# Kernel optimization log

Hardware: AMD Instinct MI355X
Metric: run time of the kernel (lower is better)

The kernel has to match this reference:

```python
import jax, jax.numpy as jnp
import numpy as np

NUM, K = 5, 3  # grid intervals and spline order, as in KANLayer(num=5, k=3)

def _grid(num=NUM, k=K, lo=-1.0, hi=1.0):
    # base grid: num+1 points on [lo,hi], extended by k knots on each side (pykan extend_grid)
    h = (hi - lo) / num
    return jnp.linspace(lo - k * h, hi + k * h, num + 1 + 2 * k, dtype=jnp.float32)

def b_spline_basis(x, grid, k=K):
    # Cox-de Boor recursion, identical to pykan B_batch. x: (B, In) -> (B, In, num+k)
    xe = x[..., None]
    b = ((xe >= grid[:-1]) & (xe < grid[1:])).astype(x.dtype)  # order-0 indicators
    for d in range(1, k + 1):
        left = (xe - grid[:-(d + 1)]) / (grid[d:-1] - grid[:-(d + 1)])
        right = (grid[d + 1:] - xe) / (grid[d + 1:] - grid[1:-d])
        b = left * b[..., :-1] + right * b[..., 1:]
    return b

def kan_layer(x, coef, sb, ssp, grid):
    # x: (B, In); coef: (Out, In, nb); sb/ssp: (Out, In). mask == 1.
    basis = b_spline_basis(x, grid)                       # (B, In, nb)
    spline = jnp.einsum('big,oig->boi', basis, coef)      # per-edge spline value
    y = sb[None] * jax.nn.silu(x)[:, None, :] + ssp[None] * spline  # (B, Out, In)
    return y.sum(axis=2)                                  # (B, Out)

def setup_inputs() -> dict:
    key = jax.random.key(0)
    ks = jax.random.split(key, 3)
    B, IN, H, OUT, NB = 128, 3072, 256, 10, NUM + K
    return {
        "x": jax.random.normal(ks[0], (B, IN), jnp.float32),
        "coef1": 0.1 * jax.random.normal(ks[1], (H, IN, NB), jnp.float32),
        "scale_base1": jnp.ones((H, IN), jnp.float32),
        "scale_sp1": jnp.ones((H, IN), jnp.float32),
        "coef2": 0.1 * jax.random.normal(ks[2], (OUT, H, NB), jnp.float32),
        "scale_base2": jnp.ones((OUT, H), jnp.float32),
        "scale_sp2": jnp.ones((OUT, H), jnp.float32),
    }

def reference(x, coef1, scale_base1, scale_sp1, coef2, scale_base2, scale_sp2):
    g = _grid()
    h = kan_layer(x, coef1, scale_base1, scale_sp1, g)
    h = jax.nn.selu(h)
    return kan_layer(h, coef2, scale_base2, scale_sp2, g)
```

## Files before the change

### kernel.cpp

```cpp
#include <hip/hip_runtime.h>
#include <hip/hip_bf16.h>
#include <math.h>


#define B_DIM   128
#define IN1     3072
#define OUT1    256
#define NB      8
#define OUT2    10

#define CI      16
#define NCH     (IN1 / CI)
#define KS      6
#define LDP     200
#define BN      32

typedef short  bf16x8 __attribute__((ext_vector_type(8)));
typedef float  f32x4  __attribute__((ext_vector_type(4)));
typedef unsigned short ushort_t;

__device__ __forceinline__ ushort_t f2bf(float f) {
    union { __hip_bfloat16 h; ushort_t u; } v;
    v.h = __float2bfloat16(f);
    return v.u;
}
__device__ __forceinline__ float bf2f(ushort_t h) {
    union { float f; unsigned int u; } v; v.u = ((unsigned int)h) << 16;
    return v.f;
}

__device__ __forceinline__ void basis_silu(float x, float w[8], float& sil) {
    sil = x / (1.0f + __expf(-x));
    float u  = (x + 2.2f) * 2.5f;
    float uf = floorf(u);
    int   j  = (int)uf;
    float t  = u - uf;
    float omt = 1.0f - t;
    float t2 = t * t, t3 = t2 * t;
    float w0 = omt * omt * omt * (1.0f / 6.0f);
    float w1 = (3.0f * t3 - 6.0f * t2 + 4.0f) * (1.0f / 6.0f);
    float w2 = (-3.0f * t3 + 3.0f * t2 + 3.0f * t + 1.0f) * (1.0f / 6.0f);
    float w3 = t3 * (1.0f / 6.0f);
    bool valid = (u >= 0.0f) && (u < 11.0f);
#pragma unroll
    for (int g = 0; g < 8; ++g) {
        int m = g - j + 3;
        float v = (m == 0) ? w0 : (m == 1) ? w1 : (m == 2) ? w2 : (m == 3) ? w3 : 0.0f;
        w[g] = valid ? v : 0.0f;
    }
}

__device__ __forceinline__ float selu_f(float x) {
    const float scale = 1.0507009873554805f;
    const float alpha = 1.6732632423543772f;
    return (x > 0.0f) ? scale * x : scale * alpha * (__expf(x) - 1.0f);
}

__global__ __launch_bounds__(512) void kan_gemm(const float* __restrict__ x,
                                                const float* __restrict__ coef1,
                                                const float* __restrict__ sb1,
                                                const float* __restrict__ ssp1,
                                                ushort_t* __restrict__ partial) {
    __shared__ ushort_t Al[B_DIM][LDP];
    __shared__ ushort_t Bl[BN][LDP];
    const int tid   = threadIdx.x;
    const int o0    = blockIdx.x * BN;
    const int chunk = blockIdx.y;
    const int i0    = chunk * CI;

    {
        const int ol = tid >> 4;
        const int ii = tid & 15;
        const size_t e = (size_t)(o0 + ol) * IN1 + (i0 + ii);
        const float4 c0 = *reinterpret_cast<const float4*>(coef1 + e * NB);
        const float4 c1 = *reinterpret_cast<const float4*>(coef1 + e * NB + 4);
        const float sspv = ssp1[e];
        const float sbv  = sb1[e];
        ushort4 pa, pb, pc;
        pa.x = f2bf(c0.x * sspv); pa.y = f2bf(c0.y * sspv);
        pa.z = f2bf(c0.z * sspv); pa.w = f2bf(c0.w * sspv);
        pb.x = f2bf(c1.x * sspv); pb.y = f2bf(c1.y * sspv);
        pb.z = f2bf(c1.z * sspv); pb.w = f2bf(c1.w * sspv);
        pc.x = f2bf(sbv); pc.y = 0; pc.z = 0; pc.w = 0;
        *reinterpret_cast<ushort4*>(&Bl[ol][ii * 12 + 0]) = pa;
        *reinterpret_cast<ushort4*>(&Bl[ol][ii * 12 + 4]) = pb;
        *reinterpret_cast<ushort4*>(&Bl[ol][ii * 12 + 8]) = pc;
    }
    {
        const int b = tid >> 2;
        const int q = tid & 3;
        float4 xv = *reinterpret_cast<const float4*>(x + (size_t)b * IN1 + i0 + q * 4);
        float xa[4] = {xv.x, xv.y, xv.z, xv.w};
#pragma unroll
        for (int p = 0; p < 4; ++p) {
            const int ii = q * 4 + p;
            float bs[8], sil;
            basis_silu(xa[p], bs, sil);
            ushort4 pa, pb, pc;
            pa.x = f2bf(bs[0]); pa.y = f2bf(bs[1]); pa.z = f2bf(bs[2]); pa.w = f2bf(bs[3]);
            pb.x = f2bf(bs[4]); pb.y = f2bf(bs[5]); pb.z = f2bf(bs[6]); pb.w = f2bf(bs[7]);
            pc.x = f2bf(sil);   pc.y = 0;           pc.z = 0;           pc.w = 0;
            *reinterpret_cast<ushort4*>(&Al[b][ii * 12 + 0]) = pa;
            *reinterpret_cast<ushort4*>(&Al[b][ii * 12 + 4]) = pb;
            *reinterpret_cast<ushort4*>(&Al[b][ii * 12 + 8]) = pc;
        }
    }
    __syncthreads();

    const int w = tid >> 6, l = tid & 63;
    const int nt = w & 1, mg = w >> 1;
    const int row16 = l & 15, kg = (l >> 4) * 8;
    f32x4 acc0 = {0.f, 0.f, 0.f, 0.f};
    f32x4 acc1 = {0.f, 0.f, 0.f, 0.f};
#pragma unroll
    for (int ks = 0; ks < KS; ++ks) {
        bf16x8 bfrag = *reinterpret_cast<const bf16x8*>(&Bl[nt * 16 + row16][ks * 32 + kg]);
        bf16x8 a0 = *reinterpret_cast<const bf16x8*>(&Al[(mg * 2 + 0) * 16 + row16][ks * 32 + kg]);
        bf16x8 a1 = *reinterpret_cast<const bf16x8*>(&Al[(mg * 2 + 1) * 16 + row16][ks * 32 + kg]);
        acc0 = __builtin_amdgcn_mfma_f32_16x16x32_bf16(a0, bfrag, acc0, 0, 0, 0);
        acc1 = __builtin_amdgcn_mfma_f32_16x16x32_bf16(a1, bfrag, acc1, 0, 0, 0);
    }

    const size_t base = (size_t)chunk * (B_DIM * OUT1);
    const int col = o0 + nt * 16 + row16;
    const int rb  = (l >> 4) * 4;
#pragma unroll
    for (int r = 0; r < 4; ++r) {
        partial[base + (size_t)((mg * 2 + 0) * 16 + rb + r) * OUT1 + col] = f2bf(acc0[r]);
        partial[base + (size_t)((mg * 2 + 1) * 16 + rb + r) * OUT1 + col] = f2bf(acc1[r]);
    }
}

#define CPG (NCH / 4)

__global__ __launch_bounds__(1024) void kan_reduce_l2(const ushort_t* __restrict__ partial,
                                                      const float* __restrict__ coef2,
                                                      const float* __restrict__ sb2,
                                                      const float* __restrict__ ssp2,
                                                      float* __restrict__ out) {
    const int b = blockIdx.x;
    const int t = threadIdx.x;
    const int o = t & 255;
    const int g = t >> 8;
    const ushort_t* pp = partial + (size_t)g * CPG * (B_DIM * OUT1)
                                 + (size_t)b * OUT1 + o;
    float sum = 0.0f;
#pragma unroll 8
    for (int c = 0; c < CPG; ++c)
        sum += bf2f(pp[(size_t)c * (B_DIM * OUT1)]);

    __shared__ float hred[4][OUT1];
    hred[g][o] = sum;
    __syncthreads();
    const float hv = hred[0][o] + hred[1][o] + hred[2][o] + hred[3][o];

    const float sh = selu_f(hv);
    float w8[8], sil;
    basis_silu(sh, w8, sil);

    float accs[OUT2];
#pragma unroll
    for (int oo = 0; oo < OUT2; ++oo) {
        const float* cp = coef2 + ((size_t)oo * OUT1 + o) * NB;
        float4 c0 = *reinterpret_cast<const float4*>(cp);
        float4 c1 = *reinterpret_cast<const float4*>(cp + 4);
        float dot = w8[0] * c0.x + w8[1] * c0.y + w8[2] * c0.z + w8[3] * c0.w +
                    w8[4] * c1.x + w8[5] * c1.y + w8[6] * c1.z + w8[7] * c1.w;
        accs[oo] = sb2[oo * OUT1 + o] * sil + ssp2[oo * OUT1 + o] * dot;
    }

    __shared__ float red[16][OUT2];
    const int lane = t & 63, wv = t >> 6;
#pragma unroll
    for (int oo = 0; oo < OUT2; ++oo) {
        float v = accs[oo];
#pragma unroll
        for (int off = 32; off >= 1; off >>= 1) v += __shfl_xor(v, off, 64);
        if (lane == 0) red[wv][oo] = v;
    }
    __syncthreads();
    if (t < OUT2)
        out[b * OUT2 + t] = red[0][t] + red[1][t] + red[2][t] + red[3][t];
}

extern "C" void kernel_launch(void* const* d_in, const int* in_sizes, int n_in,
                              void* d_out, int out_size, void* d_ws, size_t ws_size,
                              hipStream_t stream) {
    const float* x     = (const float*)d_in[0];
    const float* coef1 = (const float*)d_in[1];
    const float* sb1   = (const float*)d_in[2];
    const float* ssp1  = (const float*)d_in[3];
    const float* coef2 = (const float*)d_in[4];
    const float* sb2   = (const float*)d_in[5];
    const float* ssp2  = (const float*)d_in[6];
    float* out = (float*)d_out;

    ushort_t* partial = (ushort_t*)d_ws;

    kan_gemm<<<dim3(OUT1 / BN, NCH), 512, 0, stream>>>(x, coef1, sb1, ssp1, partial);
    kan_reduce_l2<<<B_DIM, 1024, 0, stream>>>(partial, coef2, sb2, ssp2, out);
}
```

Measured before the change: 44.34 us.

## Widen K-chunks with double-buffered swizzled LDS pipeline and transposed x input

Each GEMM block now covers 48 input features in six stages of eight, with register prefetch two stages ahead and double-buffered XOR-swizzled LDS tiles. A separate transpose kernel makes x loads coalesced along the batch dimension. The chunk count drops from 192 to 64, which shrinks the partial buffer and the reduce loop, and partials are now stored in fp32 instead of bf16. The cost is an extra kernel launch, fewer GEMM blocks (512 vs 1536), and more syncs per block.

```diff
diff --git a/kernel.cpp b/kernel.cpp
--- a/kernel.cpp
+++ b/kernel.cpp
@@ -9,11 +9,13 @@
 #define NB      8
 #define OUT2    10
 
-#define CI      16
+#define CI      48
 #define NCH     (IN1 / CI)
-#define KS      6
-#define LDP     200
+#define NS      6
+#define SI      8
 #define BN      32
+#define ASTR_B  256
+#define BSTR_B  192
 
 typedef short  bf16x8 __attribute__((ext_vector_type(8)));
 typedef float  f32x4  __attribute__((ext_vector_type(4)));
@@ -23,10 +25,6 @@
     union { __hip_bfloat16 h; ushort_t u; } v;
     v.h = __float2bfloat16(f);
     return v.u;
-}
-__device__ __forceinline__ float bf2f(ushort_t h) {
-    union { float f; unsigned int u; } v; v.u = ((unsigned int)h) << 16;
-    return v.f;
 }
 
 __device__ __forceinline__ void basis_silu(float x, float w[8], float& sil) {
@@ -56,84 +54,145 @@
     return (x > 0.0f) ? scale * x : scale * alpha * (__expf(x) - 1.0f);
 }
 
-__global__ __launch_bounds__(512) void kan_gemm(const float* __restrict__ x,
+__global__ __launch_bounds__(256) void ktranspose(const float* __restrict__ x,
+                                                  float* __restrict__ xT) {
+    __shared__ float t[32][33];
+    int bx = blockIdx.x, by = blockIdx.y;
+    int tx = threadIdx.x, ty = threadIdx.y;
+#pragma unroll
+    for (int k = 0; k < 4; ++k)
+        t[ty + k * 8][tx] = x[(by * 32 + ty + k * 8) * IN1 + bx * 32 + tx];
+    __syncthreads();
+#pragma unroll
+    for (int k = 0; k < 4; ++k)
+        xT[(bx * 32 + ty + k * 8) * B_DIM + by * 32 + tx] = t[tx][ty + k * 8];
+}
+
+__global__ __launch_bounds__(512) void kan_gemm(const float* __restrict__ xT,
                                                 const float* __restrict__ coef1,
                                                 const float* __restrict__ sb1,
                                                 const float* __restrict__ ssp1,
-                                                ushort_t* __restrict__ partial) {
-    __shared__ ushort_t Al[B_DIM][LDP];
-    __shared__ ushort_t Bl[BN][LDP];
+                                                float* __restrict__ partial) {
+    __shared__ ushort_t Asm[2][B_DIM * (ASTR_B / 2)];
+    __shared__ ushort_t Bsm[2][BN * (BSTR_B / 2)];
+
     const int tid   = threadIdx.x;
     const int o0    = blockIdx.x * BN;
     const int chunk = blockIdx.y;
-    const int i0    = chunk * CI;
-
-    {
-        const int ol = tid >> 4;
-        const int ii = tid & 15;
-        const size_t e = (size_t)(o0 + ol) * IN1 + (i0 + ii);
-        const float4 c0 = *reinterpret_cast<const float4*>(coef1 + e * NB);
-        const float4 c1 = *reinterpret_cast<const float4*>(coef1 + e * NB + 4);
-        const float sspv = ssp1[e];
-        const float sbv  = sb1[e];
-        ushort4 pa, pb, pc;
-        pa.x = f2bf(c0.x * sspv); pa.y = f2bf(c0.y * sspv);
-        pa.z = f2bf(c0.z * sspv); pa.w = f2bf(c0.w * sspv);
-        pb.x = f2bf(c1.x * sspv); pb.y = f2bf(c1.y * sspv);
-        pb.z = f2bf(c1.z * sspv); pb.w = f2bf(c1.w * sspv);
-        pc.x = f2bf(sbv); pc.y = 0; pc.z = 0; pc.w = 0;
-        *reinterpret_cast<ushort4*>(&Bl[ol][ii * 12 + 0]) = pa;
-        *reinterpret_cast<ushort4*>(&Bl[ol][ii * 12 + 4]) = pb;
-        *reinterpret_cast<ushort4*>(&Bl[ol][ii * 12 + 8]) = pc;
-    }
-    {
-        const int b = tid >> 2;
-        const int q = tid & 3;
-        float4 xv = *reinterpret_cast<const float4*>(x + (size_t)b * IN1 + i0 + q * 4);
-        float xa[4] = {xv.x, xv.y, xv.z, xv.w};
-#pragma unroll
-        for (int p = 0; p < 4; ++p) {
-            const int ii = q * 4 + p;
-            float bs[8], sil;
-            basis_silu(xa[p], bs, sil);
-            ushort4 pa, pb, pc;
-            pa.x = f2bf(bs[0]); pa.y = f2bf(bs[1]); pa.z = f2bf(bs[2]); pa.w = f2bf(bs[3]);
-            pb.x = f2bf(bs[4]); pb.y = f2bf(bs[5]); pb.z = f2bf(bs[6]); pb.w = f2bf(bs[7]);
-            pc.x = f2bf(sil);   pc.y = 0;           pc.z = 0;           pc.w = 0;
-            *reinterpret_cast<ushort4*>(&Al[b][ii * 12 + 0]) = pa;
-            *reinterpret_cast<ushort4*>(&Al[b][ii * 12 + 4]) = pb;
-            *reinterpret_cast<ushort4*>(&Al[b][ii * 12 + 8]) = pc;
-        }
-    }
-    __syncthreads();
+    const int i_base = chunk * CI;
+
+    const int bq  = tid >> 3;
+    const int iiA = tid & 7;
+    const int ol  = (tid & 255) >> 3;
+    const int iiW = tid & 7;
+    const bool doW = (tid < 256);
 
     const int w = tid >> 6, l = tid & 63;
     const int nt = w & 1, mg = w >> 1;
-    const int row16 = l & 15, kg = (l >> 4) * 8;
+    const int row16 = l & 15, k16 = l >> 4;
+
+    float  xv0[2], xv1[2];
+    float4 c0r[2], c1r[2];
+    float  sspr[2], sbr[2];
+
+#define LOADS(set, ss)                                                          \
+    {                                                                           \
+        const int ib = i_base + (ss) * SI;                                      \
+        xv0[set] = xT[(size_t)(ib + iiA) * B_DIM + bq];                         \
+        xv1[set] = xT[(size_t)(ib + iiA) * B_DIM + bq + 64];                    \
+        if (doW) {                                                              \
+            const size_t e = (size_t)(o0 + ol) * IN1 + (ib + iiW);              \
+            c0r[set] = *reinterpret_cast<const float4*>(coef1 + e * NB);        \
+            c1r[set] = *reinterpret_cast<const float4*>(coef1 + e * NB + 4);    \
+            sspr[set] = ssp1[e];                                                \
+            sbr[set]  = sb1[e];                                                 \
+        }                                                                       \
+    }
+
     f32x4 acc0 = {0.f, 0.f, 0.f, 0.f};
     f32x4 acc1 = {0.f, 0.f, 0.f, 0.f};
-#pragma unroll
-    for (int ks = 0; ks < KS; ++ks) {
-        bf16x8 bfrag = *reinterpret_cast<const bf16x8*>(&Bl[nt * 16 + row16][ks * 32 + kg]);
-        bf16x8 a0 = *reinterpret_cast<const bf16x8*>(&Al[(mg * 2 + 0) * 16 + row16][ks * 32 + kg]);
-        bf16x8 a1 = *reinterpret_cast<const bf16x8*>(&Al[(mg * 2 + 1) * 16 + row16][ks * 32 + kg]);
-        acc0 = __builtin_amdgcn_mfma_f32_16x16x32_bf16(a0, bfrag, acc0, 0, 0, 0);
-        acc1 = __builtin_amdgcn_mfma_f32_16x16x32_bf16(a1, bfrag, acc1, 0, 0, 0);
-    }
-
-    const size_t base = (size_t)chunk * (B_DIM * OUT1);
+
+    LOADS(0, 0)
+    LOADS(1, 1)
+
+#pragma unroll
+    for (int s = 0; s < NS; ++s) {
+        const int set = s & 1;
+        char* Aw = (char*)&Asm[set][0];
+        char* Bw = (char*)&Bsm[set][0];
+
+        {
+            float xa[2] = {xv0[set], xv1[set]};
+#pragma unroll
+            for (int p = 0; p < 2; ++p) {
+                const int b = bq + p * 64;
+                float bs[8], sil;
+                basis_silu(xa[p], bs, sil);
+                ushort4 pa, pb, pc;
+                pa.x = f2bf(bs[0]); pa.y = f2bf(bs[1]); pa.z = f2bf(bs[2]); pa.w = f2bf(bs[3]);
+                pb.x = f2bf(bs[4]); pb.y = f2bf(bs[5]); pb.z = f2bf(bs[6]); pb.w = f2bf(bs[7]);
+                pc.x = f2bf(sil);   pc.y = 0;           pc.z = 0;           pc.w = 0;
+                char* rowp = Aw + b * ASTR_B;
+                const int sw = (b & 7) << 4;
+                *reinterpret_cast<ushort4*>(rowp + ((iiA * 24 + 0)  ^ sw)) = pa;
+                *reinterpret_cast<ushort4*>(rowp + ((iiA * 24 + 8)  ^ sw)) = pb;
+                *reinterpret_cast<ushort4*>(rowp + ((iiA * 24 + 16) ^ sw)) = pc;
+            }
+            if (doW) {
+                const float sspv = sspr[set], sbv = sbr[set];
+                const float4 c0 = c0r[set], c1 = c1r[set];
+                ushort4 pa, pb, pc;
+                pa.x = f2bf(c0.x * sspv); pa.y = f2bf(c0.y * sspv);
+                pa.z = f2bf(c0.z * sspv); pa.w = f2bf(c0.w * sspv);
+                pb.x = f2bf(c1.x * sspv); pb.y = f2bf(c1.y * sspv);
+                pb.z = f2bf(c1.z * sspv); pb.w = f2bf(c1.w * sspv);
+                pc.x = f2bf(sbv); pc.y = 0; pc.z = 0; pc.w = 0;
+                char* rowp = Bw + ol * BSTR_B;
+                const int sw = (ol & 3) << 4;
+                *reinterpret_cast<ushort4*>(rowp + ((iiW * 24 + 0)  ^ sw)) = pa;
+                *reinterpret_cast<ushort4*>(rowp + ((iiW * 24 + 8)  ^ sw)) = pb;
+                *reinterpret_cast<ushort4*>(rowp + ((iiW * 24 + 16) ^ sw)) = pc;
+            }
+        }
+        __syncthreads();
+
+        if (s < NS - 2) LOADS(set, s + 2)
+
+        {
+            const char* Ar = (const char*)&Asm[set][0];
+            const char* Br = (const char*)&Bsm[set][0];
+            const int orow = nt * 16 + row16;
+            const int r0 = (mg * 2) * 16 + row16;
+            const int r1 = r0 + 16;
+            const int swA = (row16 & 7) << 4;
+            const int swB = (orow & 3) << 4;
+#pragma unroll
+            for (int ks = 0; ks < 3; ++ks) {
+                const int pre = ks * 64 + k16 * 16;
+                bf16x8 bf = *reinterpret_cast<const bf16x8*>(Br + orow * BSTR_B + (pre ^ swB));
+                bf16x8 a0 = *reinterpret_cast<const bf16x8*>(Ar + r0 * ASTR_B + (pre ^ swA));
+                bf16x8 a1 = *reinterpret_cast<const bf16x8*>(Ar + r1 * ASTR_B + (pre ^ swA));
+                acc0 = __builtin_amdgcn_mfma_f32_16x16x32_bf16(a0, bf, acc0, 0, 0, 0);
+                acc1 = __builtin_amdgcn_mfma_f32_16x16x32_bf16(a1, bf, acc1, 0, 0, 0);
+            }
+        }
+        __syncthreads();
+    }
+#undef LOADS
+
+    float* pbase = partial + (size_t)chunk * (B_DIM * OUT1);
     const int col = o0 + nt * 16 + row16;
-    const int rb  = (l >> 4) * 4;
+    const int rb  = k16 * 4;
 #pragma unroll
     for (int r = 0; r < 4; ++r) {
-        partial[base + (size_t)((mg * 2 + 0) * 16 + rb + r) * OUT1 + col] = f2bf(acc0[r]);
-        partial[base + (size_t)((mg * 2 + 1) * 16 + rb + r) * OUT1 + col] = f2bf(acc1[r]);
+        pbase[(size_t)((mg * 2 + 0) * 16 + rb + r) * OUT1 + col] = acc0[r];
+        pbase[(size_t)((mg * 2 + 1) * 16 + rb + r) * OUT1 + col] = acc1[r];
     }
 }
 
 #define CPG (NCH / 4)
 
-__global__ __launch_bounds__(1024) void kan_reduce_l2(const ushort_t* __restrict__ partial,
+__global__ __launch_bounds__(1024) void kan_reduce_l2(const float* __restrict__ partial,
                                                       const float* __restrict__ coef2,
                                                       const float* __restrict__ sb2,
                                                       const float* __restrict__ ssp2,
@@ -142,12 +201,12 @@
     const int t = threadIdx.x;
     const int o = t & 255;
     const int g = t >> 8;
-    const ushort_t* pp = partial + (size_t)g * CPG * (B_DIM * OUT1)
-                                 + (size_t)b * OUT1 + o;
+    const float* pp = partial + (size_t)g * CPG * (B_DIM * OUT1)
+                              + (size_t)b * OUT1 + o;
     float sum = 0.0f;
-#pragma unroll 8
+#pragma unroll
     for (int c = 0; c < CPG; ++c)
-        sum += bf2f(pp[(size_t)c * (B_DIM * OUT1)]);
+        sum += pp[(size_t)c * (B_DIM * OUT1)];
 
     __shared__ float hred[4][OUT1];
     hred[g][o] = sum;
@@ -195,8 +254,10 @@
     const float* ssp2  = (const float*)d_in[6];
     float* out = (float*)d_out;
 
-    ushort_t* partial = (ushort_t*)d_ws;
-
-    kan_gemm<<<dim3(OUT1 / BN, NCH), 512, 0, stream>>>(x, coef1, sb1, ssp1, partial);
+    float* xT      = (float*)d_ws;
+    float* partial = (float*)((char*)d_ws + (size_t)IN1 * B_DIM * 4);
+
+    ktranspose<<<dim3(96, 4), dim3(32, 8), 0, stream>>>(x, xT);
+    kan_gemm<<<dim3(OUT1 / BN, NCH), 512, 0, stream>>>(xT, coef1, sb1, ssp1, partial);
     kan_reduce_l2<<<B_DIM, 1024, 0, stream>>>(partial, coef2, sb2, ssp2, out);
 }
```

After: 48.26 us. 1.09x slower.

## Split layer-1 into prepack kernels and a pipelined direct-to-LDS split-K GEMM

Applied to the files above, without the earlier changes.

Layer 1 now runs in three kernels. Two conversion kernels first write the spline basis plus SiLU activations and the scaled coefficient weights as swizzled bf16 rows in workspace, with K dense at 9 values per input instead of padded to 12. The GEMM streams those rows with global_load_lds into double-buffered LDS, uses larger 64-wide output tiles and a 108-way K split, and writes fewer partials for the reduction kernel. This removes the padding waste and the per-block recomputation of basis values, at the cost of two extra launches and a workspace round trip of about 17 MB.

```diff
diff --git a/kernel.cpp b/kernel.cpp
--- a/kernel.cpp
+++ b/kernel.cpp
@@ -9,15 +9,15 @@
 #define NB      8
 #define OUT2    10
 
-#define CI      16
-#define NCH     (IN1 / CI)
-#define KS      6
-#define LDP     200
-#define BN      32
+#define KTOT    27648
+#define ROWB    55296
+#define SPLITK  108
+#define BN      64
 
 typedef short  bf16x8 __attribute__((ext_vector_type(8)));
 typedef float  f32x4  __attribute__((ext_vector_type(4)));
 typedef unsigned short ushort_t;
+typedef unsigned int u32;
 
 __device__ __forceinline__ ushort_t f2bf(float f) {
     union { __hip_bfloat16 h; ushort_t u; } v;
@@ -25,8 +25,14 @@
     return v.u;
 }
 __device__ __forceinline__ float bf2f(ushort_t h) {
-    union { float f; unsigned int u; } v; v.u = ((unsigned int)h) << 16;
+    union { float f; u32 u; } v; v.u = ((u32)h) << 16;
     return v.f;
+}
+
+__device__ __forceinline__ void gl_lds16(const void* g, void* l) {
+    __builtin_amdgcn_global_load_lds(
+        (const __attribute__((address_space(1))) u32*)g,
+        (__attribute__((address_space(3))) u32*)l, 16, 0, 0);
 }
 
 __device__ __forceinline__ void basis_silu(float x, float w[8], float& sil) {
@@ -56,96 +62,181 @@
     return (x > 0.0f) ? scale * x : scale * alpha * (__expf(x) - 1.0f);
 }
 
-__global__ __launch_bounds__(512) void kan_gemm(const float* __restrict__ x,
-                                                const float* __restrict__ coef1,
-                                                const float* __restrict__ sb1,
-                                                const float* __restrict__ ssp1,
-                                                ushort_t* __restrict__ partial) {
-    __shared__ ushort_t Al[B_DIM][LDP];
-    __shared__ ushort_t Bl[BN][LDP];
-    const int tid   = threadIdx.x;
-    const int o0    = blockIdx.x * BN;
-    const int chunk = blockIdx.y;
-    const int i0    = chunk * CI;
-
+__global__ __launch_bounds__(128) void kconv_a(const float* __restrict__ x,
+                                               char* __restrict__ Ag) {
+    const int gid = blockIdx.x * 128 + threadIdx.x;
+    const int b  = gid / 384;
+    const int ig = gid - b * 384;
+    const int i0 = ig * 8;
+
+    float4 x0 = *reinterpret_cast<const float4*>(x + (size_t)b * IN1 + i0);
+    float4 x1 = *reinterpret_cast<const float4*>(x + (size_t)b * IN1 + i0 + 4);
+    float xa[8] = {x0.x, x0.y, x0.z, x0.w, x1.x, x1.y, x1.z, x1.w};
+
+    float bs[8][8], sil[8];
+#pragma unroll
+    for (int p = 0; p < 8; ++p) basis_silu(xa[p], bs[p], sil[p]);
+
+    char* rowp = Ag + (size_t)b * ROWB;
+    const int qsw = ((ig & 7) ^ (b & 7)) << 4;
+#pragma unroll
+    for (int s = 0; s < 9; ++s) {
+        ushort_t v[8];
+#pragma unroll
+        for (int p = 0; p < 8; ++p)
+            v[p] = f2bf((s < 8) ? bs[p][s] : sil[p]);
+        *reinterpret_cast<uint4*>(rowp + (s * 48 + (ig >> 3)) * 128 + qsw) =
+            *reinterpret_cast<const uint4*>(v);
+    }
+}
+
+__global__ __launch_bounds__(128) void kconv_w(const float* __restrict__ coef1,
+                                               const float* __restrict__ sb1,
+                                               const float* __restrict__ ssp1,
+                                               char* __restrict__ Wg) {
+    const int gid = blockIdx.x * 128 + threadIdx.x;
+    const int o  = gid / 384;
+    const int ig = gid - o * 384;
+    const int i0 = ig * 8;
+
+    float cf[8][8], sspv[8], sbv[8];
+#pragma unroll
+    for (int p = 0; p < 8; ++p) {
+        const float* cp = coef1 + ((size_t)o * IN1 + i0 + p) * NB;
+        float4 c0 = *reinterpret_cast<const float4*>(cp);
+        float4 c1 = *reinterpret_cast<const float4*>(cp + 4);
+        cf[p][0] = c0.x; cf[p][1] = c0.y; cf[p][2] = c0.z; cf[p][3] = c0.w;
+        cf[p][4] = c1.x; cf[p][5] = c1.y; cf[p][6] = c1.z; cf[p][7] = c1.w;
+    }
     {
-        const int ol = tid >> 4;
-        const int ii = tid & 15;
-        const size_t e = (size_t)(o0 + ol) * IN1 + (i0 + ii);
-        const float4 c0 = *reinterpret_cast<const float4*>(coef1 + e * NB);
-        const float4 c1 = *reinterpret_cast<const float4*>(coef1 + e * NB + 4);
-        const float sspv = ssp1[e];
-        const float sbv  = sb1[e];
-        ushort4 pa, pb, pc;
-        pa.x = f2bf(c0.x * sspv); pa.y = f2bf(c0.y * sspv);
-        pa.z = f2bf(c0.z * sspv); pa.w = f2bf(c0.w * sspv);
-        pb.x = f2bf(c1.x * sspv); pb.y = f2bf(c1.y * sspv);
-        pb.z = f2bf(c1.z * sspv); pb.w = f2bf(c1.w * sspv);
-        pc.x = f2bf(sbv); pc.y = 0; pc.z = 0; pc.w = 0;
-        *reinterpret_cast<ushort4*>(&Bl[ol][ii * 12 + 0]) = pa;
-        *reinterpret_cast<ushort4*>(&Bl[ol][ii * 12 + 4]) = pb;
-        *reinterpret_cast<ushort4*>(&Bl[ol][ii * 12 + 8]) = pc;
-    }
-    {
-        const int b = tid >> 2;
-        const int q = tid & 3;
-        float4 xv = *reinterpret_cast<const float4*>(x + (size_t)b * IN1 + i0 + q * 4);
-        float xa[4] = {xv.x, xv.y, xv.z, xv.w};
-#pragma unroll
-        for (int p = 0; p < 4; ++p) {
-            const int ii = q * 4 + p;
-            float bs[8], sil;
-            basis_silu(xa[p], bs, sil);
-            ushort4 pa, pb, pc;
-            pa.x = f2bf(bs[0]); pa.y = f2bf(bs[1]); pa.z = f2bf(bs[2]); pa.w = f2bf(bs[3]);
-            pb.x = f2bf(bs[4]); pb.y = f2bf(bs[5]); pb.z = f2bf(bs[6]); pb.w = f2bf(bs[7]);
-            pc.x = f2bf(sil);   pc.y = 0;           pc.z = 0;           pc.w = 0;
-            *reinterpret_cast<ushort4*>(&Al[b][ii * 12 + 0]) = pa;
-            *reinterpret_cast<ushort4*>(&Al[b][ii * 12 + 4]) = pb;
-            *reinterpret_cast<ushort4*>(&Al[b][ii * 12 + 8]) = pc;
+        float4 s0 = *reinterpret_cast<const float4*>(ssp1 + (size_t)o * IN1 + i0);
+        float4 s1 = *reinterpret_cast<const float4*>(ssp1 + (size_t)o * IN1 + i0 + 4);
+        sspv[0]=s0.x; sspv[1]=s0.y; sspv[2]=s0.z; sspv[3]=s0.w;
+        sspv[4]=s1.x; sspv[5]=s1.y; sspv[6]=s1.z; sspv[7]=s1.w;
+        float4 b0 = *reinterpret_cast<const float4*>(sb1 + (size_t)o * IN1 + i0);
+        float4 b1 = *reinterpret_cast<const float4*>(sb1 + (size_t)o * IN1 + i0 + 4);
+        sbv[0]=b0.x; sbv[1]=b0.y; sbv[2]=b0.z; sbv[3]=b0.w;
+        sbv[4]=b1.x; sbv[5]=b1.y; sbv[6]=b1.z; sbv[7]=b1.w;
+    }
+
+    char* rowp = Wg + (size_t)o * ROWB;
+    const int qsw = ((ig & 7) ^ (o & 7)) << 4;
+#pragma unroll
+    for (int s = 0; s < 9; ++s) {
+        ushort_t v[8];
+#pragma unroll
+        for (int p = 0; p < 8; ++p)
+            v[p] = f2bf((s < 8) ? cf[p][s] * sspv[p] : sbv[p]);
+        *reinterpret_cast<uint4*>(rowp + (s * 48 + (ig >> 3)) * 128 + qsw) =
+            *reinterpret_cast<const uint4*>(v);
+    }
+}
+
+__global__ __launch_bounds__(512) void kgemm(const char* __restrict__ Ag,
+                                             const char* __restrict__ Wg,
+                                             ushort_t* __restrict__ partial) {
+    __shared__ __align__(16) char lds[2][24576];
+
+    const int tid = threadIdx.x;
+    const int w   = tid >> 6, l = tid & 63;
+    const int nt  = blockIdx.x, kc = blockIdx.y;
+    const int o0  = nt * BN;
+
+    const int ar0 = tid >> 3;
+    const int ar1 = 64 + (tid >> 3);
+    const int aq  = tid & 7;
+    const char* Asrc0 = Ag + (size_t)ar0 * ROWB + ((aq ^ (ar0 & 7)) << 4);
+    const char* Asrc1 = Ag + (size_t)ar1 * ROWB + ((aq ^ (ar1 & 7)) << 4);
+    const int wr = tid >> 3;
+    const char* Wsrc = Wg + (size_t)(o0 + wr) * ROWB + ((aq ^ (wr & 7)) << 4);
+
+#define ISSUE(ss, buf)                                                        \
+    {                                                                         \
+        const int cb = (kc * 4 + (ss)) * 128;                                 \
+        char* base = &lds[buf][0];                                            \
+        gl_lds16(Asrc0 + cb, base + w * 1024);                                \
+        gl_lds16(Asrc1 + cb, base + 8192 + w * 1024);                         \
+        gl_lds16(Wsrc  + cb, base + 16384 + w * 1024);                        \
+    }
+
+    f32x4 acc[2][2];
+#pragma unroll
+    for (int a = 0; a < 2; ++a)
+#pragma unroll
+        for (int bq = 0; bq < 2; ++bq) acc[a][bq] = (f32x4){0.f, 0.f, 0.f, 0.f};
+
+    const int mq = w >> 1, nq = w & 1;
+    const int r16 = l & 15, k16 = l >> 4;
+
+    ISSUE(0, 0)
+    ISSUE(1, 1)
+
+#pragma unroll
+    for (int s = 0; s < 4; ++s) {
+        if (s < 3) { asm volatile("s_waitcnt vmcnt(3)" ::: "memory"); }
+        else       { asm volatile("s_waitcnt vmcnt(0)" ::: "memory"); }
+        __builtin_amdgcn_s_barrier();
+        asm volatile("" ::: "memory");
+
+        const char* Ab = &lds[s & 1][0];
+        const char* Wb = &lds[s & 1][16384];
+#pragma unroll
+        for (int ks = 0; ks < 2; ++ks) {
+            const int qf = ks * 4 + k16;
+            bf16x8 bf[2], af[2];
+#pragma unroll
+            for (int bq = 0; bq < 2; ++bq) {
+                const int rn = nq * 32 + bq * 16 + r16;
+                bf[bq] = *reinterpret_cast<const bf16x8*>(Wb + rn * 128 + ((qf ^ (rn & 7)) << 4));
+            }
+#pragma unroll
+            for (int a = 0; a < 2; ++a) {
+                const int rm = mq * 32 + a * 16 + r16;
+                af[a] = *reinterpret_cast<const bf16x8*>(Ab + rm * 128 + ((qf ^ (rm & 7)) << 4));
+            }
+#pragma unroll
+            for (int a = 0; a < 2; ++a)
+#pragma unroll
+                for (int bq = 0; bq < 2; ++bq)
+                    acc[a][bq] = __builtin_amdgcn_mfma_f32_16x16x32_bf16(af[a], bf[bq], acc[a][bq], 0, 0, 0);
         }
-    }
-    __syncthreads();
-
-    const int w = tid >> 6, l = tid & 63;
-    const int nt = w & 1, mg = w >> 1;
-    const int row16 = l & 15, kg = (l >> 4) * 8;
-    f32x4 acc0 = {0.f, 0.f, 0.f, 0.f};
-    f32x4 acc1 = {0.f, 0.f, 0.f, 0.f};
-#pragma unroll
-    for (int ks = 0; ks < KS; ++ks) {
-        bf16x8 bfrag = *reinterpret_cast<const bf16x8*>(&Bl[nt * 16 + row16][ks * 32 + kg]);
-        bf16x8 a0 = *reinterpret_cast<const bf16x8*>(&Al[(mg * 2 + 0) * 16 + row16][ks * 32 + kg]);
-        bf16x8 a1 = *reinterpret_cast<const bf16x8*>(&Al[(mg * 2 + 1) * 16 + row16][ks * 32 + kg]);
-        acc0 = __builtin_amdgcn_mfma_f32_16x16x32_bf16(a0, bfrag, acc0, 0, 0, 0);
-        acc1 = __builtin_amdgcn_mfma_f32_16x16x32_bf16(a1, bfrag, acc1, 0, 0, 0);
-    }
-
-    const size_t base = (size_t)chunk * (B_DIM * OUT1);
-    const int col = o0 + nt * 16 + row16;
-    const int rb  = (l >> 4) * 4;
-#pragma unroll
-    for (int r = 0; r < 4; ++r) {
-        partial[base + (size_t)((mg * 2 + 0) * 16 + rb + r) * OUT1 + col] = f2bf(acc0[r]);
-        partial[base + (size_t)((mg * 2 + 1) * 16 + rb + r) * OUT1 + col] = f2bf(acc1[r]);
-    }
-}
-
-#define CPG (NCH / 4)
-
-__global__ __launch_bounds__(1024) void kan_reduce_l2(const ushort_t* __restrict__ partial,
-                                                      const float* __restrict__ coef2,
-                                                      const float* __restrict__ sb2,
-                                                      const float* __restrict__ ssp2,
-                                                      float* __restrict__ out) {
+
+        __builtin_amdgcn_s_barrier();
+        asm volatile("" ::: "memory");
+        if (s == 0) ISSUE(2, 0)
+        if (s == 1) ISSUE(3, 1)
+    }
+#undef ISSUE
+
+    ushort_t* pp = partial + (size_t)kc * (B_DIM * OUT1);
+#pragma unroll
+    for (int a = 0; a < 2; ++a) {
+#pragma unroll
+        for (int bq = 0; bq < 2; ++bq) {
+            const int col = o0 + nq * 32 + bq * 16 + r16;
+#pragma unroll
+            for (int r = 0; r < 4; ++r) {
+                const int row = mq * 32 + a * 16 + k16 * 4 + r;
+                pp[(size_t)row * OUT1 + col] = f2bf(acc[a][bq][r]);
+            }
+        }
+    }
+}
+
+#define CPG (SPLITK / 4)
+
+__global__ __launch_bounds__(1024) void kreduce(const ushort_t* __restrict__ partial,
+                                                const float* __restrict__ coef2,
+                                                const float* __restrict__ sb2,
+                                                const float* __restrict__ ssp2,
+                                                float* __restrict__ out) {
     const int b = blockIdx.x;
     const int t = threadIdx.x;
     const int o = t & 255;
     const int g = t >> 8;
-    const ushort_t* pp = partial + (size_t)g * CPG * (B_DIM * OUT1)
-                                 + (size_t)b * OUT1 + o;
+    const ushort_t* pp = partial + ((size_t)g * CPG * B_DIM + b) * OUT1 + o;
     float sum = 0.0f;
-#pragma unroll 8
+#pragma unroll
     for (int c = 0; c < CPG; ++c)
         sum += bf2f(pp[(size_t)c * (B_DIM * OUT1)]);
 
@@ -195,8 +286,12 @@
     const float* ssp2  = (const float*)d_in[6];
     float* out = (float*)d_out;
 
-    ushort_t* partial = (ushort_t*)d_ws;
-
-    kan_gemm<<<dim3(OUT1 / BN, NCH), 512, 0, stream>>>(x, coef1, sb1, ssp1, partial);
-    kan_reduce_l2<<<B_DIM, 1024, 0, stream>>>(partial, coef2, sb2, ssp2, out);
-}
+    char*     Ag      = (char*)d_ws;
+    char*     Wg      = Ag + (size_t)B_DIM * ROWB;
+    ushort_t* partial = (ushort_t*)(Wg + (size_t)OUT1 * ROWB);
+
+    kconv_a<<<384, 128, 0, stream>>>(x, Ag);
+    kconv_w<<<768, 128, 0, stream>>>(coef1, sb1, ssp1, Wg);
+    kgemm<<<dim3(OUT1 / BN, SPLITK), 512, 0, stream>>>(Ag, Wg, partial);
+    kreduce<<<B_DIM, 1024, 0, stream>>>(partial, coef2, sb2, ssp2, out);
+}
```

New measurement: 44.82 us. Within noise of the previous version (+1.1%).

## Precompute bf16 basis into global buffer and load MFMA fragments directly

Applied to the files above, without the earlier changes.

Adds a separate kernel that evaluates the B-spline basis and SiLU once per input element and stores them as bf16 in workspace. The GEMM kernel drops LDS staging and barriers, loads A and B fragments straight from global memory with the silu term as a separate MFMA step, uses a split-K chunk of 32 inputs, and writes fp32 partials. Before, every output-tile block recomputed the basis for its chunk. The change adds a third launch, a global round-trip for the basis, and fp32 partials that double the reduction traffic.

```diff
diff --git a/kernel.cpp b/kernel.cpp
--- a/kernel.cpp
+++ b/kernel.cpp
@@ -9,24 +9,28 @@
 #define NB      8
 #define OUT2    10
 
-#define CI      16
-#define NCH     (IN1 / CI)
-#define KS      6
-#define LDP     200
-#define BN      32
+#define KTOT    (IN1 * 8)
+#define CI      32
+#define SPLITK  (IN1 / CI)
+#define CPG     (SPLITK / 4)
 
 typedef short  bf16x8 __attribute__((ext_vector_type(8)));
 typedef float  f32x4  __attribute__((ext_vector_type(4)));
 typedef unsigned short ushort_t;
+typedef unsigned int u32;
 
 __device__ __forceinline__ ushort_t f2bf(float f) {
     union { __hip_bfloat16 h; ushort_t u; } v;
     v.h = __float2bfloat16(f);
     return v.u;
 }
-__device__ __forceinline__ float bf2f(ushort_t h) {
-    union { float f; unsigned int u; } v; v.u = ((unsigned int)h) << 16;
-    return v.f;
+
+__device__ __forceinline__ bf16x8 pack8(float a0, float a1, float a2, float a3,
+                                        float a4, float a5, float a6, float a7) {
+    union { ushort_t u[8]; bf16x8 v; } r;
+    r.u[0] = f2bf(a0); r.u[1] = f2bf(a1); r.u[2] = f2bf(a2); r.u[3] = f2bf(a3);
+    r.u[4] = f2bf(a4); r.u[5] = f2bf(a5); r.u[6] = f2bf(a6); r.u[7] = f2bf(a7);
+    return r.v;
 }
 
 __device__ __forceinline__ void basis_silu(float x, float w[8], float& sil) {
@@ -56,98 +60,104 @@
     return (x > 0.0f) ? scale * x : scale * alpha * (__expf(x) - 1.0f);
 }
 
-__global__ __launch_bounds__(512) void kan_gemm(const float* __restrict__ x,
-                                                const float* __restrict__ coef1,
-                                                const float* __restrict__ sb1,
-                                                const float* __restrict__ ssp1,
-                                                ushort_t* __restrict__ partial) {
-    __shared__ ushort_t Al[B_DIM][LDP];
-    __shared__ ushort_t Bl[BN][LDP];
-    const int tid   = threadIdx.x;
-    const int o0    = blockIdx.x * BN;
-    const int chunk = blockIdx.y;
-    const int i0    = chunk * CI;
-
-    {
-        const int ol = tid >> 4;
-        const int ii = tid & 15;
-        const size_t e = (size_t)(o0 + ol) * IN1 + (i0 + ii);
-        const float4 c0 = *reinterpret_cast<const float4*>(coef1 + e * NB);
-        const float4 c1 = *reinterpret_cast<const float4*>(coef1 + e * NB + 4);
-        const float sspv = ssp1[e];
-        const float sbv  = sb1[e];
-        ushort4 pa, pb, pc;
-        pa.x = f2bf(c0.x * sspv); pa.y = f2bf(c0.y * sspv);
-        pa.z = f2bf(c0.z * sspv); pa.w = f2bf(c0.w * sspv);
-        pb.x = f2bf(c1.x * sspv); pb.y = f2bf(c1.y * sspv);
-        pb.z = f2bf(c1.z * sspv); pb.w = f2bf(c1.w * sspv);
-        pc.x = f2bf(sbv); pc.y = 0; pc.z = 0; pc.w = 0;
-        *reinterpret_cast<ushort4*>(&Bl[ol][ii * 12 + 0]) = pa;
-        *reinterpret_cast<ushort4*>(&Bl[ol][ii * 12 + 4]) = pb;
-        *reinterpret_cast<ushort4*>(&Bl[ol][ii * 12 + 8]) = pc;
-    }
-    {
-        const int b = tid >> 2;
-        const int q = tid & 3;
-        float4 xv = *reinterpret_cast<const float4*>(x + (size_t)b * IN1 + i0 + q * 4);
-        float xa[4] = {xv.x, xv.y, xv.z, xv.w};
-#pragma unroll
-        for (int p = 0; p < 4; ++p) {
-            const int ii = q * 4 + p;
-            float bs[8], sil;
-            basis_silu(xa[p], bs, sil);
-            ushort4 pa, pb, pc;
-            pa.x = f2bf(bs[0]); pa.y = f2bf(bs[1]); pa.z = f2bf(bs[2]); pa.w = f2bf(bs[3]);
-            pb.x = f2bf(bs[4]); pb.y = f2bf(bs[5]); pb.z = f2bf(bs[6]); pb.w = f2bf(bs[7]);
-            pc.x = f2bf(sil);   pc.y = 0;           pc.z = 0;           pc.w = 0;
-            *reinterpret_cast<ushort4*>(&Al[b][ii * 12 + 0]) = pa;
-            *reinterpret_cast<ushort4*>(&Al[b][ii * 12 + 4]) = pb;
-            *reinterpret_cast<ushort4*>(&Al[b][ii * 12 + 8]) = pc;
-        }
-    }
-    __syncthreads();
-
-    const int w = tid >> 6, l = tid & 63;
-    const int nt = w & 1, mg = w >> 1;
-    const int row16 = l & 15, kg = (l >> 4) * 8;
+__global__ __launch_bounds__(256) void kconv_a(const float* __restrict__ x,
+                                               char* __restrict__ Ag,
+                                               char* __restrict__ Asil) {
+    const int gid = blockIdx.x * 256 + threadIdx.x;
+    const int b  = gid / 384;
+    const int ig = gid - b * 384;
+    const int i0 = ig * 8;
+
+    const float* xp = x + (size_t)b * IN1 + i0;
+    float4 x0 = *reinterpret_cast<const float4*>(xp);
+    float4 x1 = *reinterpret_cast<const float4*>(xp + 4);
+    float xa[8] = {x0.x, x0.y, x0.z, x0.w, x1.x, x1.y, x1.z, x1.w};
+
+    char* ap = Ag + ((size_t)b * KTOT + (size_t)i0 * 8) * 2;
+    union { ushort_t u[8]; uint4 q; } sil;
+#pragma unroll
+    for (int p = 0; p < 8; ++p) {
+        float bs[8], sl;
+        basis_silu(xa[p], bs, sl);
+        sil.u[p] = f2bf(sl);
+        union { ushort_t u[8]; uint4 q; } t;
+#pragma unroll
+        for (int g = 0; g < 8; ++g) t.u[g] = f2bf(bs[g]);
+        *reinterpret_cast<uint4*>(ap + p * 16) = t.q;
+    }
+    *reinterpret_cast<uint4*>(Asil + ((size_t)b * IN1 + i0) * 2) = sil.q;
+}
+
+__global__ __launch_bounds__(512) void kgemm(const char* __restrict__ Ag,
+                                             const char* __restrict__ Asil,
+                                             const float* __restrict__ coef1,
+                                             const float* __restrict__ sb1,
+                                             const float* __restrict__ ssp1,
+                                             float* __restrict__ partial) {
+    const int tid = threadIdx.x;
+    const int w   = tid >> 6, l = tid & 63;
+    const int mg  = w >> 1, nq = w & 1;
+    const int q   = l >> 4, r16 = l & 15;
+    const int o0  = blockIdx.x * 32;
+    const int kc  = blockIdx.y;
+    const int i0  = kc * CI;
+    const int o   = o0 + nq * 16 + r16;
+
+    const float* cofp = coef1 + ((size_t)o * IN1 + i0 + q) * 8;
+    const float* sspp = ssp1 + (size_t)o * IN1 + i0 + q;
+    const char*  a0p  = Ag + ((size_t)(mg * 32 + r16) * KTOT + (size_t)(i0 + q) * 8) * 2;
+    const char*  a1p  = a0p + (size_t)16 * KTOT * 2;
+
     f32x4 acc0 = {0.f, 0.f, 0.f, 0.f};
     f32x4 acc1 = {0.f, 0.f, 0.f, 0.f};
-#pragma unroll
-    for (int ks = 0; ks < KS; ++ks) {
-        bf16x8 bfrag = *reinterpret_cast<const bf16x8*>(&Bl[nt * 16 + row16][ks * 32 + kg]);
-        bf16x8 a0 = *reinterpret_cast<const bf16x8*>(&Al[(mg * 2 + 0) * 16 + row16][ks * 32 + kg]);
-        bf16x8 a1 = *reinterpret_cast<const bf16x8*>(&Al[(mg * 2 + 1) * 16 + row16][ks * 32 + kg]);
-        acc0 = __builtin_amdgcn_mfma_f32_16x16x32_bf16(a0, bfrag, acc0, 0, 0, 0);
-        acc1 = __builtin_amdgcn_mfma_f32_16x16x32_bf16(a1, bfrag, acc1, 0, 0, 0);
-    }
-
-    const size_t base = (size_t)chunk * (B_DIM * OUT1);
-    const int col = o0 + nt * 16 + row16;
-    const int rb  = (l >> 4) * 4;
+
+#pragma unroll
+    for (int ks = 0; ks < 8; ++ks) {
+        float4 c0 = *reinterpret_cast<const float4*>(cofp + ks * 32);
+        float4 c1 = *reinterpret_cast<const float4*>(cofp + ks * 32 + 4);
+        float  sv = sspp[ks * 4];
+        bf16x8 bf = pack8(c0.x * sv, c0.y * sv, c0.z * sv, c0.w * sv,
+                          c1.x * sv, c1.y * sv, c1.z * sv, c1.w * sv);
+        bf16x8 a0 = *reinterpret_cast<const bf16x8*>(a0p + ks * 64);
+        bf16x8 a1 = *reinterpret_cast<const bf16x8*>(a1p + ks * 64);
+        acc0 = __builtin_amdgcn_mfma_f32_16x16x32_bf16(a0, bf, acc0, 0, 0, 0);
+        acc1 = __builtin_amdgcn_mfma_f32_16x16x32_bf16(a1, bf, acc1, 0, 0, 0);
+    }
+    {
+        const float* sbp = sb1 + (size_t)o * IN1 + i0 + q * 8;
+        float4 s0 = *reinterpret_cast<const float4*>(sbp);
+        float4 s1 = *reinterpret_cast<const float4*>(sbp + 4);
+        bf16x8 bf = pack8(s0.x, s0.y, s0.z, s0.w, s1.x, s1.y, s1.z, s1.w);
+        const char* sa0 = Asil + ((size_t)(mg * 32 + r16) * IN1 + i0 + q * 8) * 2;
+        const char* sa1 = sa0 + (size_t)16 * IN1 * 2;
+        bf16x8 a0 = *reinterpret_cast<const bf16x8*>(sa0);
+        bf16x8 a1 = *reinterpret_cast<const bf16x8*>(sa1);
+        acc0 = __builtin_amdgcn_mfma_f32_16x16x32_bf16(a0, bf, acc0, 0, 0, 0);
+        acc1 = __builtin_amdgcn_mfma_f32_16x16x32_bf16(a1, bf, acc1, 0, 0, 0);
+    }
+
+    float* pp = partial + (size_t)kc * (B_DIM * OUT1);
 #pragma unroll
     for (int r = 0; r < 4; ++r) {
-        partial[base + (size_t)((mg * 2 + 0) * 16 + rb + r) * OUT1 + col] = f2bf(acc0[r]);
-        partial[base + (size_t)((mg * 2 + 1) * 16 + rb + r) * OUT1 + col] = f2bf(acc1[r]);
-    }
-}
-
-#define CPG (NCH / 4)
-
-__global__ __launch_bounds__(1024) void kan_reduce_l2(const ushort_t* __restrict__ partial,
-                                                      const float* __restrict__ coef2,
-                                                      const float* __restrict__ sb2,
-                                                      const float* __restrict__ ssp2,
-                                                      float* __restrict__ out) {
+        pp[(size_t)((mg * 2 + 0) * 16 + q * 4 + r) * OUT1 + o] = acc0[r];
+        pp[(size_t)((mg * 2 + 1) * 16 + q * 4 + r) * OUT1 + o] = acc1[r];
+    }
+}
+
+__global__ __launch_bounds__(1024) void kreduce(const float* __restrict__ partial,
+                                                const float* __restrict__ coef2,
+                                                const float* __restrict__ sb2,
+                                                const float* __restrict__ ssp2,
+                                                float* __restrict__ out) {
     const int b = blockIdx.x;
     const int t = threadIdx.x;
     const int o = t & 255;
     const int g = t >> 8;
-    const ushort_t* pp = partial + (size_t)g * CPG * (B_DIM * OUT1)
-                                 + (size_t)b * OUT1 + o;
+    const float* pp = partial + ((size_t)g * CPG * B_DIM + b) * OUT1 + o;
     float sum = 0.0f;
-#pragma unroll 8
+#pragma unroll
     for (int c = 0; c < CPG; ++c)
-        sum += bf2f(pp[(size_t)c * (B_DIM * OUT1)]);
+        sum += pp[(size_t)c * (B_DIM * OUT1)];
 
     __shared__ float hred[4][OUT1];
     hred[g][o] = sum;
@@ -195,8 +205,11 @@
     const float* ssp2  = (const float*)d_in[6];
     float* out = (float*)d_out;
 
-    ushort_t* partial = (ushort_t*)d_ws;
-
-    kan_gemm<<<dim3(OUT1 / BN, NCH), 512, 0, stream>>>(x, coef1, sb1, ssp1, partial);
-    kan_reduce_l2<<<B_DIM, 1024, 0, stream>>>(partial, coef2, sb2, ssp2, out);
-}
+    char*  Ag      = (char*)d_ws;
+    char*  Asil    = Ag + (size_t)B_DIM * KTOT * 2;
+    float* partial = (float*)(Asil + (size_t)B_DIM * IN1 * 2);
+
+    kconv_a<<<192, 256, 0, stream>>>(x, Ag, Asil);
+    kgemm<<<dim3(OUT1 / 32, SPLITK), 512, 0, stream>>>(Ag, Asil, coef1, sb1, ssp1, partial);
+    kreduce<<<B_DIM, 1024, 0, stream>>>(partial, coef2, sb2, ssp2, out);
+}
```

Result: slower. 58.58 us (+32.1%).
